# Optimization experiments

Measured on AMD Instinct MI355X. Metric: run time of the kernel, lower is better.

The kernel has to match this reference:

```python
import jax, jax.numpy as jnp
import numpy as np

B = 1 << 21          # shading points per batch
U_RES, CH = 400, 8   # spatial plane
A_RES, ACH = 50, 50 and 8  # placeholder, real consts below
A_RES, ACH = 50, 8   # angular planes (h/d)
HID = 32
IN_CH = CH + 2 * ACH  # 24


def _bilerp_clamp(tex, uv):
    # Bilinear interp, both axes clamped (U-plane). tex: (H,W,C), uv: (B,2) in [0,1]
    H, W, _ = tex.shape
    u = jnp.clip(uv[:, 0], 0.0, 1.0) * (W - 1)
    v = jnp.clip(uv[:, 1], 0.0, 1.0) * (H - 1)
    x0 = jnp.floor(u).astype(jnp.int32)
    x1 = jnp.clip(x0 + 1, 0, W - 1)
    y0 = jnp.floor(v).astype(jnp.int32)
    y1 = jnp.clip(y0 + 1, 0, H - 1)
    ur = (u - x0.astype(u.dtype))[:, None]
    vr = (v - y0.astype(v.dtype))[:, None]
    p00 = tex[y0, x0]; p10 = tex[y0, x1]; p01 = tex[y1, x0]; p11 = tex[y1, x1]
    return ((1 - ur) * (1 - vr) * p00 + ur * (1 - vr) * p10
            + (1 - ur) * vr * p01 + ur * vr * p11)


def _bilerp_wrap_u(tex, uv):
    # Bilinear interp wrapping the u (phi) axis, clamping v (H/D planes).
    H, W, _ = tex.shape
    u = (uv[:, 0] % 1.0) * W
    v = jnp.clip(uv[:, 1], 0.0, 1.0) * (H - 1)
    x0f = jnp.floor(u)
    x0 = x0f.astype(jnp.int32) % W
    x1 = (x0 + 1) % W
    y0 = jnp.floor(v).astype(jnp.int32)
    y1 = jnp.clip(y0 + 1, 0, H - 1)
    ur = (u - x0f)[:, None]
    vr = (v - y0.astype(v.dtype))[:, None]
    p00 = tex[y0, x0]; p10 = tex[y0, x1]; p01 = tex[y1, x0]; p11 = tex[y1, x1]
    return ((1 - ur) * (1 - vr) * p00 + ur * (1 - vr) * p10
            + (1 - ur) * vr * p01 + ur * vr * p11)


def setup_inputs() -> dict:
    key = jax.random.key(0)
    ks = jax.random.split(key, 8)
    x = jax.random.uniform(ks[0], (B, 6), dtype=jnp.float32)
    u_plane = 0.01 * jax.random.normal(ks[1], (U_RES, U_RES, CH), dtype=jnp.float32)
    h_plane = 0.01 * jax.random.normal(ks[2], (A_RES, A_RES, ACH), dtype=jnp.float32)
    d_plane = 0.01 * jax.random.normal(ks[3], (A_RES, A_RES, ACH), dtype=jnp.float32)
    def lin_w(k, fout, fin):  # torch nn.Linear default init (kaiming-uniform-ish)
        lim = 1.0 / np.sqrt(fin)
        return jax.random.uniform(k, (fout, fin), jnp.float32, -lim, lim)
    W0 = lin_w(ks[4], HID, IN_CH)
    W1 = lin_w(ks[5], HID, HID)
    W2 = lin_w(ks[6], HID, HID)
    W3 = lin_w(ks[7], 3, HID)
    return {"x": x, "u_plane": u_plane, "h_plane": h_plane, "d_plane": d_plane,
            "W0": W0, "W1": W1, "W2": W2, "W3": W3}


def reference(x, u_plane, h_plane, d_plane, W0, W1, W2, W3):
    # Split and reorder: H/D planes receive (u=phi, v=theta)
    uv = x[:, 0:2]
    h_uv = jnp.stack((x[:, 3], x[:, 2]), axis=1)
    d_uv = jnp.stack((x[:, 5], x[:, 4]), axis=1)
    fU = _bilerp_clamp(u_plane, uv)       # (B, CH)
    fH = _bilerp_wrap_u(h_plane, h_uv)    # (B, ACH)
    fD = _bilerp_wrap_u(d_plane, d_uv)    # (B, ACH)
    feat = jnp.concatenate([fU, fH, fD], axis=1)  # (B, 24)
    # Quant mode 'off' -> QLinear is a plain bias-free matmul with W^T
    h = jax.nn.relu(feat @ W0.T)
    h = jax.nn.relu(h @ W1.T)
    h = jax.nn.relu(h @ W2.T)
    return h @ W3.T  # (B, 3)
```

## Files before the change

kernel.cpp:

```cpp
#include <hip/hip_runtime.h>

typedef _Float16 half4 __attribute__((ext_vector_type(4)));
typedef _Float16 half8 __attribute__((ext_vector_type(8)));
typedef float floatx4 __attribute__((ext_vector_type(4)));

#define U_RESV 400
#define A_RESV 50

#define UHALVES (U_RESV * U_RESV * 8)
#define AHALVES (A_RESV * A_RESV * 8)
#define WOFF    (UHALVES + 2 * AHALVES)
#define W0OFF   0
#define W1OFF   896
#define W2OFF   2048
#define W3OFF   3200
#define WTOT    3776

__device__ __forceinline__ float clamp01(float x) { return fminf(fmaxf(x, 0.0f), 1.0f); }

__device__ __forceinline__ floatx4 mfma16(half4 a, half4 b, floatx4 c) {
    return __builtin_amdgcn_mfma_f32_16x16x16f16(a, b, c, 0, 0, 0);
}
__device__ __forceinline__ half4 zero4() {
    half4 h; h[0] = h[1] = h[2] = h[3] = (_Float16)0.f; return h;
}
__device__ __forceinline__ half4 relu4(half4 v) {
#if __has_builtin(__builtin_elementwise_max)
    return __builtin_elementwise_max(v, zero4());
#else
    half4 r;
#pragma unroll
    for (int i = 0; i < 4; ++i) r[i] = v[i] > (_Float16)0.f ? v[i] : (_Float16)0.f;
    return r;
#endif
}

__device__ __forceinline__ void cvt_chunk(const float* __restrict__ src,
                                          _Float16* __restrict__ dst, int i) {
    float4 a = *(const float4*)(src + (size_t)i * 8);
    float4 b = *(const float4*)(src + (size_t)i * 8 + 4);
    half8 h;
    h[0] = (_Float16)a.x; h[1] = (_Float16)a.y; h[2] = (_Float16)a.z; h[3] = (_Float16)a.w;
    h[4] = (_Float16)b.x; h[5] = (_Float16)b.y; h[6] = (_Float16)b.z; h[7] = (_Float16)b.w;
    *(half8*)(dst + (size_t)i * 8) = h;
}

__device__ __forceinline__ void wblob_fill(const float* __restrict__ W0,
                                           const float* __restrict__ W1,
                                           const float* __restrict__ W2,
                                           const float* __restrict__ W3,
                                           _Float16* __restrict__ w, int tid, int nthr) {
    for (int i = tid; i < WTOT; i += nthr) {
        float v;
        if (i < W1OFF) {
            int r = i / 28, c = i - r * 28;
            v = (c < 24) ? W0[r * 24 + c] : 0.f;
        } else if (i < W2OFF) {
            int j = i - W1OFF, r = j / 36, c = j - r * 36;
            v = (c < 32) ? W1[r * 32 + c] : 0.f;
        } else if (i < W3OFF) {
            int j = i - W2OFF, r = j / 36, c = j - r * 36;
            v = (c < 32) ? W2[r * 32 + c] : 0.f;
        } else {
            int j = i - W3OFF, r = j / 36, c = j - r * 36;
            v = (r < 3 && c < 32) ? W3[r * 32 + c] : 0.f;
        }
        w[i] = (_Float16)v;
    }
}

__global__ __launch_bounds__(256) void pconv_kernel(
    const float* __restrict__ u_plane, const float* __restrict__ h_plane,
    const float* __restrict__ d_plane, const float* __restrict__ W0,
    const float* __restrict__ W1, const float* __restrict__ W2,
    const float* __restrict__ W3, _Float16* __restrict__ dst) {
    const int gid = blockIdx.x * 256 + threadIdx.x;
    const int gsz = gridDim.x * 256;
    for (int i = gid; i < UHALVES / 8; i += gsz) cvt_chunk(u_plane, dst, i);
    for (int i = gid; i < AHALVES / 8; i += gsz) cvt_chunk(h_plane, dst + UHALVES, i);
    for (int i = gid; i < AHALVES / 8; i += gsz) cvt_chunk(d_plane, dst + UHALVES + AHALVES, i);
    if (blockIdx.x == 0) wblob_fill(W0, W1, W2, W3, dst + WOFF, threadIdx.x, 256);
}

__global__ __launch_bounds__(256) void wprep_kernel(
    const float* __restrict__ W0, const float* __restrict__ W1,
    const float* __restrict__ W2, const float* __restrict__ W3,
    _Float16* __restrict__ wdst) {
    wblob_fill(W0, W1, W2, W3, wdst, threadIdx.x, 256);
}


template <bool F16P>
__global__ __launch_bounds__(512, 2) void tpmlp_kernel(
    const float* __restrict__ x,
    const void* __restrict__ u_tex,
    const void* __restrict__ h_tex,
    const void* __restrict__ d_tex,
    const _Float16* __restrict__ wsw,
    float* __restrict__ out) {
    const int tid  = threadIdx.x;
    const int lane = tid & 63;
    const int wv   = tid >> 6;
    const int q    = lane >> 4;
    const int c15  = lane & 15;

    __shared__ __align__(16) _Float16 fl[512 * 28];
    __shared__ __align__(16) _Float16 wl[WTOT];

    const size_t P = (size_t)blockIdx.x * 512 + tid;
    const float2* xp = (const float2*)(x + P * 6);
    float2 p01v = xp[0], p23v = xp[1], p45v = xp[2];

    uint4 w_a;
    if (tid < 472) w_a = ((const uint4*)wsw)[tid];

    int oU0, oU1, oU2, oU3;  float uw00, uw10, uw01, uw11;
    {
        float u = clamp01(p01v.x) * (float)(U_RESV - 1);
        float v = clamp01(p01v.y) * (float)(U_RESV - 1);
        float x0f = floorf(u), y0f = floorf(v);
        int x0 = (int)x0f, y0 = (int)y0f;
        int x1 = min(x0 + 1, U_RESV - 1), y1 = min(y0 + 1, U_RESV - 1);
        float ur = u - x0f, vr = v - y0f;
        uw00 = (1.0f - ur) * (1.0f - vr); uw10 = ur * (1.0f - vr);
        uw01 = (1.0f - ur) * vr;          uw11 = ur * vr;
        oU0 = (y0 * U_RESV + x0) * 8;
        oU1 = (y0 * U_RESV + x1) * 8;
        oU2 = (y1 * U_RESV + x0) * 8;
        oU3 = (y1 * U_RESV + x1) * 8;
    }
    int oH0, oH1, oH2, oH3;  float hw00, hw10, hw01, hw11;
    {
        float uu = p23v.y, vv = p23v.x;
        float uf = uu - floorf(uu);
        float u = uf * (float)A_RESV;
        float v = clamp01(vv) * (float)(A_RESV - 1);
        float x0f = floorf(u), y0f = floorf(v);
        int x0 = (int)x0f;
        int x1 = x0 + 1; if (x1 == A_RESV) x1 = 0;
        int y0 = (int)y0f;
        int y1 = min(y0 + 1, A_RESV - 1);
        float ur = u - x0f, vr = v - y0f;
        hw00 = (1.0f - ur) * (1.0f - vr); hw10 = ur * (1.0f - vr);
        hw01 = (1.0f - ur) * vr;          hw11 = ur * vr;
        oH0 = (y0 * A_RESV + x0) * 8;
        oH1 = (y0 * A_RESV + x1) * 8;
        oH2 = (y1 * A_RESV + x0) * 8;
        oH3 = (y1 * A_RESV + x1) * 8;
    }
    int oD0, oD1, oD2, oD3;  float dw00, dw10, dw01, dw11;
    {
        float uu = p45v.y, vv = p45v.x;
        float uf = uu - floorf(uu);
        float u = uf * (float)A_RESV;
        float v = clamp01(vv) * (float)(A_RESV - 1);
        float x0f = floorf(u), y0f = floorf(v);
        int x0 = (int)x0f;
        int x1 = x0 + 1; if (x1 == A_RESV) x1 = 0;
        int y0 = (int)y0f;
        int y1 = min(y0 + 1, A_RESV - 1);
        float ur = u - x0f, vr = v - y0f;
        dw00 = (1.0f - ur) * (1.0f - vr); dw10 = ur * (1.0f - vr);
        dw01 = (1.0f - ur) * vr;          dw11 = ur * vr;
        oD0 = (y0 * A_RESV + x0) * 8;
        oD1 = (y0 * A_RESV + x1) * 8;
        oD2 = (y1 * A_RESV + x0) * 8;
        oD3 = (y1 * A_RESV + x1) * 8;
    }

    half8 gU0, gU1, gU2, gU3, gH0, gH1, gH2, gH3, gD0, gD1, gD2, gD3;
    float4 sU0, sU1, sU2, sU3, sH0, sH1, sH2, sH3, sD0, sD1, sD2, sD3;
    float4 rU0, rU1, rU2, rU3, rH0, rH1, rH2, rH3, rD0, rD1, rD2, rD3;
    if constexpr (F16P) {
        const _Float16* up = (const _Float16*)u_tex;
        const _Float16* hp = (const _Float16*)h_tex;
        const _Float16* dp = (const _Float16*)d_tex;
        gU0 = *(const half8*)(up + oU0);
        gU1 = *(const half8*)(up + oU1);
        gU2 = *(const half8*)(up + oU2);
        gU3 = *(const half8*)(up + oU3);
        gH0 = *(const half8*)(hp + oH0);
        gH1 = *(const half8*)(hp + oH1);
        gH2 = *(const half8*)(hp + oH2);
        gH3 = *(const half8*)(hp + oH3);
        gD0 = *(const half8*)(dp + oD0);
        gD1 = *(const half8*)(dp + oD1);
        gD2 = *(const half8*)(dp + oD2);
        gD3 = *(const half8*)(dp + oD3);
    } else {
        const float* up = (const float*)u_tex;
        const float* hp = (const float*)h_tex;
        const float* dp = (const float*)d_tex;
        sU0 = *(const float4*)(up + oU0); rU0 = *(const float4*)(up + oU0 + 4);
        sU1 = *(const float4*)(up + oU1); rU1 = *(const float4*)(up + oU1 + 4);
        sU2 = *(const float4*)(up + oU2); rU2 = *(const float4*)(up + oU2 + 4);
        sU3 = *(const float4*)(up + oU3); rU3 = *(const float4*)(up + oU3 + 4);
        sH0 = *(const float4*)(hp + oH0); rH0 = *(const float4*)(hp + oH0 + 4);
        sH1 = *(const float4*)(hp + oH1); rH1 = *(const float4*)(hp + oH1 + 4);
        sH2 = *(const float4*)(hp + oH2); rH2 = *(const float4*)(hp + oH2 + 4);
        sH3 = *(const float4*)(hp + oH3); rH3 = *(const float4*)(hp + oH3 + 4);
        sD0 = *(const float4*)(dp + oD0); rD0 = *(const float4*)(dp + oD0 + 4);
        sD1 = *(const float4*)(dp + oD1); rD1 = *(const float4*)(dp + oD1 + 4);
        sD2 = *(const float4*)(dp + oD2); rD2 = *(const float4*)(dp + oD2 + 4);
        sD3 = *(const float4*)(dp + oD3); rD3 = *(const float4*)(dp + oD3 + 4);
    }
    __builtin_amdgcn_sched_barrier(0);

    if (tid < 472) ((uint4*)wl)[tid] = w_a;
    asm volatile("s_waitcnt lgkmcnt(0)" ::: "memory");
    __builtin_amdgcn_s_barrier();

    float fU[8], fH[8], fD[8];
    if constexpr (F16P) {
#pragma unroll
        for (int i = 0; i < 8; ++i) {
            float r = (float)gU0[i] * uw00;
            r = fmaf((float)gU1[i], uw10, r);
            r = fmaf((float)gU2[i], uw01, r);
            r = fmaf((float)gU3[i], uw11, r);
            fU[i] = r;
        }
#pragma unroll
        for (int i = 0; i < 8; ++i) {
            float r = (float)gH0[i] * hw00;
            r = fmaf((float)gH1[i], hw10, r);
            r = fmaf((float)gH2[i], hw01, r);
            r = fmaf((float)gH3[i], hw11, r);
            fH[i] = r;
        }
#pragma unroll
        for (int i = 0; i < 8; ++i) {
            float r = (float)gD0[i] * dw00;
            r = fmaf((float)gD1[i], dw10, r);
            r = fmaf((float)gD2[i], dw01, r);
            r = fmaf((float)gD3[i], dw11, r);
            fD[i] = r;
        }
    } else {
        const float* a;
        const float* b;
        const float* c;
        const float* d;
#pragma unroll
        for (int i = 0; i < 8; ++i) {
            a = i < 4 ? (const float*)&sU0 : (const float*)&rU0;
            b = i < 4 ? (const float*)&sU1 : (const float*)&rU1;
            c = i < 4 ? (const float*)&sU2 : (const float*)&rU2;
            d = i < 4 ? (const float*)&sU3 : (const float*)&rU3;
            int k = i & 3;
            float r = a[k] * uw00;
            r = fmaf(b[k], uw10, r);
            r = fmaf(c[k], uw01, r);
            r = fmaf(d[k], uw11, r);
            fU[i] = r;
        }
#pragma unroll
        for (int i = 0; i < 8; ++i) {
            a = i < 4 ? (const float*)&sH0 : (const float*)&rH0;
            b = i < 4 ? (const float*)&sH1 : (const float*)&rH1;
            c = i < 4 ? (const float*)&sH2 : (const float*)&rH2;
            d = i < 4 ? (const float*)&sH3 : (const float*)&rH3;
            int k = i & 3;
            float r = a[k] * hw00;
            r = fmaf(b[k], hw10, r);
            r = fmaf(c[k], hw01, r);
            r = fmaf(d[k], hw11, r);
            fH[i] = r;
        }
#pragma unroll
        for (int i = 0; i < 8; ++i) {
            a = i < 4 ? (const float*)&sD0 : (const float*)&rD0;
            b = i < 4 ? (const float*)&sD1 : (const float*)&rD1;
            c = i < 4 ? (const float*)&sD2 : (const float*)&rD2;
            d = i < 4 ? (const float*)&sD3 : (const float*)&rD3;
            int k = i & 3;
            float r = a[k] * dw00;
            r = fmaf(b[k], dw10, r);
            r = fmaf(c[k], dw01, r);
            r = fmaf(d[k], dw11, r);
            fD[i] = r;
        }
    }

    {
        _Float16* row = fl + tid * 28;
        half8 hU, hH, hD;
#pragma unroll
        for (int i = 0; i < 8; ++i) {
            hU[i] = (_Float16)fU[i];
            hH[i] = (_Float16)fH[i];
            hD[i] = (_Float16)fD[i];
        }
        *(half8*)(row)      = hU;
        *(half8*)(row + 8)  = hH;
        *(half8*)(row + 16) = hD;
    }
    asm volatile("s_waitcnt lgkmcnt(0)" ::: "memory");
    __builtin_amdgcn_sched_barrier(0);

    floatx4 zf; zf[0] = 0.f; zf[1] = 0.f; zf[2] = 0.f; zf[3] = 0.f;
    const _Float16* wb = fl + (size_t)wv * 64 * 28;
    const _Float16* w0l = wl + W0OFF;
    const _Float16* w1l = wl + W1OFF;
    const _Float16* w2l = wl + W2OFF;
    const _Float16* w3l = wl + W3OFF;

    half4 b0[4], b1[4];
#pragma unroll
    for (int j = 0; j < 4; ++j) {
        const _Float16* r = wb + (size_t)(j * 16 + c15) * 28;
        b0[j] = *(const half4*)(r + q * 4);
        b1[j] = (q < 2) ? *(const half4*)(r + 16 + q * 4) : zero4();
    }

    floatx4 cc[2][4];
#pragma unroll
    for (int m = 0; m < 2; ++m) {
        half4 a0 = *(const half4*)(w0l + (size_t)(16 * m + c15) * 28 + q * 4);
        half4 a1 = (q < 2) ? *(const half4*)(w0l + (size_t)(16 * m + c15) * 28 + 16 + q * 4) : zero4();
#pragma unroll
        for (int j = 0; j < 4; ++j)
            cc[m][j] = mfma16(a1, b1[j], mfma16(a0, b0[j], zf));
    }
#pragma unroll
    for (int j = 0; j < 4; ++j) {
#pragma unroll
        for (int e = 0; e < 4; ++e) {
            b0[j][e] = (_Float16)cc[0][j][e];
            b1[j][e] = (_Float16)cc[1][j][e];
        }
        b0[j] = relu4(b0[j]);
        b1[j] = relu4(b1[j]);
    }

#pragma unroll
    for (int m = 0; m < 2; ++m) {
        half4 a0 = *(const half4*)(w1l + (size_t)(16 * m + c15) * 36 + q * 4);
        half4 a1 = *(const half4*)(w1l + (size_t)(16 * m + c15) * 36 + 16 + q * 4);
#pragma unroll
        for (int j = 0; j < 4; ++j)
            cc[m][j] = mfma16(a1, b1[j], mfma16(a0, b0[j], zf));
    }
#pragma unroll
    for (int j = 0; j < 4; ++j) {
#pragma unroll
        for (int e = 0; e < 4; ++e) {
            b0[j][e] = (_Float16)cc[0][j][e];
            b1[j][e] = (_Float16)cc[1][j][e];
        }
        b0[j] = relu4(b0[j]);
        b1[j] = relu4(b1[j]);
    }

#pragma unroll
    for (int m = 0; m < 2; ++m) {
        half4 a0 = *(const half4*)(w2l + (size_t)(16 * m + c15) * 36 + q * 4);
        half4 a1 = *(const half4*)(w2l + (size_t)(16 * m + c15) * 36 + 16 + q * 4);
#pragma unroll
        for (int j = 0; j < 4; ++j)
            cc[m][j] = mfma16(a1, b1[j], mfma16(a0, b0[j], zf));
    }
#pragma unroll
    for (int j = 0; j < 4; ++j) {
#pragma unroll
        for (int e = 0; e < 4; ++e) {
            b0[j][e] = (_Float16)cc[0][j][e];
            b1[j][e] = (_Float16)cc[1][j][e];
        }
        b0[j] = relu4(b0[j]);
        b1[j] = relu4(b1[j]);
    }

    floatx4 c3[4];
    {
        half4 a0 = *(const half4*)(w3l + (size_t)c15 * 36 + q * 4);
        half4 a1 = *(const half4*)(w3l + (size_t)c15 * 36 + 16 + q * 4);
#pragma unroll
        for (int j = 0; j < 4; ++j)
            c3[j] = mfma16(a1, b1[j], mfma16(a0, b0[j], zf));
    }

    if (lane < 16) {
        const size_t base = (size_t)blockIdx.x * 512 + (size_t)wv * 64;
#pragma unroll
        for (int j = 0; j < 4; ++j) {
            size_t p = base + (size_t)j * 16 + lane;
            float* o = out + p * 3;
            o[0] = c3[j][0];
            o[1] = c3[j][1];
            o[2] = c3[j][2];
        }
    }
}

extern "C" void kernel_launch(void* const* d_in, const int* in_sizes, int n_in,
                              void* d_out, int out_size, void* d_ws, size_t ws_size,
                              hipStream_t stream) {
    const float* x       = (const float*)d_in[0];
    const float* u_plane = (const float*)d_in[1];
    const float* h_plane = (const float*)d_in[2];
    const float* d_plane = (const float*)d_in[3];
    const float* W0      = (const float*)d_in[4];
    const float* W1      = (const float*)d_in[5];
    const float* W2      = (const float*)d_in[6];
    const float* W3      = (const float*)d_in[7];
    float* out = (float*)d_out;
    _Float16* wsw = (_Float16*)d_ws;

    int n = in_sizes[0] / 6;
    int grid = n / 512;

    const size_t need = ((size_t)WOFF + WTOT) * 2;
    if (ws_size >= need) {
        pconv_kernel<<<648, 256, 0, stream>>>(u_plane, h_plane, d_plane,
                                              W0, W1, W2, W3, wsw);
        tpmlp_kernel<true><<<grid, 512, 0, stream>>>(
            x, (const void*)wsw, (const void*)(wsw + UHALVES),
            (const void*)(wsw + UHALVES + AHALVES), wsw + WOFF, out);
    } else {
        wprep_kernel<<<1, 256, 0, stream>>>(W0, W1, W2, W3, wsw);
        tpmlp_kernel<false><<<grid, 512, 0, stream>>>(
            x, (const void*)u_plane, (const void*)h_plane, (const void*)d_plane,
            wsw, out);
    }
}
```

Baseline: 72.68 us.

## Process multiple 512-point tiles per block to amortize weight staging

Each block now loops over K=4 consecutive 512-point tiles, loading the packed MLP weights into shared memory once and reusing them across iterations. The grid is reduced by 4x and launch bounds relaxed to one block per CU minimum, with gather setup factored into helper functions. This trades per-block weight load and launch overhead for fewer resident blocks and less latency hiding of the texture gathers.

```diff
diff --git a/kernel.cpp b/kernel.cpp
--- a/kernel.cpp
+++ b/kernel.cpp
@@ -89,9 +89,59 @@
     wblob_fill(W0, W1, W2, W3, wdst, threadIdx.x, 256);
 }
 
-
-template <bool F16P>
-__global__ __launch_bounds__(512, 2) void tpmlp_kernel(
+struct GA { int o0, o1, o2, o3; float w00, w10, w01, w11; };
+
+__device__ __forceinline__ GA mkU(float ux, float uy) {
+    GA g;
+    float u = clamp01(ux) * (float)(U_RESV - 1);
+    float v = clamp01(uy) * (float)(U_RESV - 1);
+    float x0f = floorf(u), y0f = floorf(v);
+    int x0 = (int)x0f, y0 = (int)y0f;
+    int x1 = min(x0 + 1, U_RESV - 1), y1 = min(y0 + 1, U_RESV - 1);
+    float ur = u - x0f, vr = v - y0f;
+    g.w00 = (1.0f - ur) * (1.0f - vr); g.w10 = ur * (1.0f - vr);
+    g.w01 = (1.0f - ur) * vr;          g.w11 = ur * vr;
+    g.o0 = (y0 * U_RESV + x0) * 8;
+    g.o1 = (y0 * U_RESV + x1) * 8;
+    g.o2 = (y1 * U_RESV + x0) * 8;
+    g.o3 = (y1 * U_RESV + x1) * 8;
+    return g;
+}
+__device__ __forceinline__ GA mkA(float uu, float vv) {
+    GA g;
+    float uf = uu - floorf(uu);
+    float u = uf * (float)A_RESV;
+    float v = clamp01(vv) * (float)(A_RESV - 1);
+    float x0f = floorf(u), y0f = floorf(v);
+    int x0 = (int)x0f;
+    int x1 = x0 + 1; if (x1 == A_RESV) x1 = 0;
+    int y0 = (int)y0f;
+    int y1 = min(y0 + 1, A_RESV - 1);
+    float ur = u - x0f, vr = v - y0f;
+    g.w00 = (1.0f - ur) * (1.0f - vr); g.w10 = ur * (1.0f - vr);
+    g.w01 = (1.0f - ur) * vr;          g.w11 = ur * vr;
+    g.o0 = (y0 * A_RESV + x0) * 8;
+    g.o1 = (y0 * A_RESV + x1) * 8;
+    g.o2 = (y1 * A_RESV + x0) * 8;
+    g.o3 = (y1 * A_RESV + x1) * 8;
+    return g;
+}
+
+__device__ __forceinline__ void blend8(half8 a, half8 b, half8 c, half8 d,
+                                       const GA& g, float* f) {
+#pragma unroll
+    for (int i = 0; i < 8; ++i) {
+        float r = (float)a[i] * g.w00;
+        r = fmaf((float)b[i], g.w10, r);
+        r = fmaf((float)c[i], g.w01, r);
+        r = fmaf((float)d[i], g.w11, r);
+        f[i] = r;
+    }
+}
+
+
+template <bool F16P, int K>
+__global__ __launch_bounds__(512, 1) void tpmlp_kernel(
     const float* __restrict__ x,
     const void* __restrict__ u_tex,
     const void* __restrict__ h_tex,
@@ -107,288 +157,219 @@
     __shared__ __align__(16) _Float16 fl[512 * 28];
     __shared__ __align__(16) _Float16 wl[WTOT];
 
-    const size_t P = (size_t)blockIdx.x * 512 + tid;
-    const float2* xp = (const float2*)(x + P * 6);
-    float2 p01v = xp[0], p23v = xp[1], p45v = xp[2];
-
-    uint4 w_a;
-    if (tid < 472) w_a = ((const uint4*)wsw)[tid];
-
-    int oU0, oU1, oU2, oU3;  float uw00, uw10, uw01, uw11;
     {
-        float u = clamp01(p01v.x) * (float)(U_RESV - 1);
-        float v = clamp01(p01v.y) * (float)(U_RESV - 1);
-        float x0f = floorf(u), y0f = floorf(v);
-        int x0 = (int)x0f, y0 = (int)y0f;
-        int x1 = min(x0 + 1, U_RESV - 1), y1 = min(y0 + 1, U_RESV - 1);
-        float ur = u - x0f, vr = v - y0f;
-        uw00 = (1.0f - ur) * (1.0f - vr); uw10 = ur * (1.0f - vr);
-        uw01 = (1.0f - ur) * vr;          uw11 = ur * vr;
-        oU0 = (y0 * U_RESV + x0) * 8;
-        oU1 = (y0 * U_RESV + x1) * 8;
-        oU2 = (y1 * U_RESV + x0) * 8;
-        oU3 = (y1 * U_RESV + x1) * 8;
+        const uint4* src = (const uint4*)wsw;
+        uint4 w_a;
+        if (tid < 472) w_a = src[tid];
+        if (tid < 472) ((uint4*)wl)[tid] = w_a;
     }
-    int oH0, oH1, oH2, oH3;  float hw00, hw10, hw01, hw11;
-    {
-        float uu = p23v.y, vv = p23v.x;
-        float uf = uu - floorf(uu);
-        float u = uf * (float)A_RESV;
-        float v = clamp01(vv) * (float)(A_RESV - 1);
-        float x0f = floorf(u), y0f = floorf(v);
-        int x0 = (int)x0f;
-        int x1 = x0 + 1; if (x1 == A_RESV) x1 = 0;
-        int y0 = (int)y0f;
-        int y1 = min(y0 + 1, A_RESV - 1);
-        float ur = u - x0f, vr = v - y0f;
-        hw00 = (1.0f - ur) * (1.0f - vr); hw10 = ur * (1.0f - vr);
-        hw01 = (1.0f - ur) * vr;          hw11 = ur * vr;
-        oH0 = (y0 * A_RESV + x0) * 8;
-        oH1 = (y0 * A_RESV + x1) * 8;
-        oH2 = (y1 * A_RESV + x0) * 8;
-        oH3 = (y1 * A_RESV + x1) * 8;
-    }
-    int oD0, oD1, oD2, oD3;  float dw00, dw10, dw01, dw11;
-    {
-        float uu = p45v.y, vv = p45v.x;
-        float uf = uu - floorf(uu);
-        float u = uf * (float)A_RESV;
-        float v = clamp01(vv) * (float)(A_RESV - 1);
-        float x0f = floorf(u), y0f = floorf(v);
-        int x0 = (int)x0f;
-        int x1 = x0 + 1; if (x1 == A_RESV) x1 = 0;
-        int y0 = (int)y0f;
-        int y1 = min(y0 + 1, A_RESV - 1);
-        float ur = u - x0f, vr = v - y0f;
-        dw00 = (1.0f - ur) * (1.0f - vr); dw10 = ur * (1.0f - vr);
-        dw01 = (1.0f - ur) * vr;          dw11 = ur * vr;
-        oD0 = (y0 * A_RESV + x0) * 8;
-        oD1 = (y0 * A_RESV + x1) * 8;
-        oD2 = (y1 * A_RESV + x0) * 8;
-        oD3 = (y1 * A_RESV + x1) * 8;
-    }
-
-    half8 gU0, gU1, gU2, gU3, gH0, gH1, gH2, gH3, gD0, gD1, gD2, gD3;
-    float4 sU0, sU1, sU2, sU3, sH0, sH1, sH2, sH3, sD0, sD1, sD2, sD3;
-    float4 rU0, rU1, rU2, rU3, rH0, rH1, rH2, rH3, rD0, rD1, rD2, rD3;
-    if constexpr (F16P) {
-        const _Float16* up = (const _Float16*)u_tex;
-        const _Float16* hp = (const _Float16*)h_tex;
-        const _Float16* dp = (const _Float16*)d_tex;
-        gU0 = *(const half8*)(up + oU0);
-        gU1 = *(const half8*)(up + oU1);
-        gU2 = *(const half8*)(up + oU2);
-        gU3 = *(const half8*)(up + oU3);
-        gH0 = *(const half8*)(hp + oH0);
-        gH1 = *(const half8*)(hp + oH1);
-        gH2 = *(const half8*)(hp + oH2);
-        gH3 = *(const half8*)(hp + oH3);
-        gD0 = *(const half8*)(dp + oD0);
-        gD1 = *(const half8*)(dp + oD1);
-        gD2 = *(const half8*)(dp + oD2);
-        gD3 = *(const half8*)(dp + oD3);
-    } else {
-        const float* up = (const float*)u_tex;
-        const float* hp = (const float*)h_tex;
-        const float* dp = (const float*)d_tex;
-        sU0 = *(const float4*)(up + oU0); rU0 = *(const float4*)(up + oU0 + 4);
-        sU1 = *(const float4*)(up + oU1); rU1 = *(const float4*)(up + oU1 + 4);
-        sU2 = *(const float4*)(up + oU2); rU2 = *(const float4*)(up + oU2 + 4);
-        sU3 = *(const float4*)(up + oU3); rU3 = *(const float4*)(up + oU3 + 4);
-        sH0 = *(const float4*)(hp + oH0); rH0 = *(const float4*)(hp + oH0 + 4);
-        sH1 = *(const float4*)(hp + oH1); rH1 = *(const float4*)(hp + oH1 + 4);
-        sH2 = *(const float4*)(hp + oH2); rH2 = *(const float4*)(hp + oH2 + 4);
-        sH3 = *(const float4*)(hp + oH3); rH3 = *(const float4*)(hp + oH3 + 4);
-        sD0 = *(const float4*)(dp + oD0); rD0 = *(const float4*)(dp + oD0 + 4);
-        sD1 = *(const float4*)(dp + oD1); rD1 = *(const float4*)(dp + oD1 + 4);
-        sD2 = *(const float4*)(dp + oD2); rD2 = *(const float4*)(dp + oD2 + 4);
-        sD3 = *(const float4*)(dp + oD3); rD3 = *(const float4*)(dp + oD3 + 4);
-    }
-    __builtin_amdgcn_sched_barrier(0);
-
-    if (tid < 472) ((uint4*)wl)[tid] = w_a;
-    asm volatile("s_waitcnt lgkmcnt(0)" ::: "memory");
-    __builtin_amdgcn_s_barrier();
-
-    float fU[8], fH[8], fD[8];
-    if constexpr (F16P) {
-#pragma unroll
-        for (int i = 0; i < 8; ++i) {
-            float r = (float)gU0[i] * uw00;
-            r = fmaf((float)gU1[i], uw10, r);
-            r = fmaf((float)gU2[i], uw01, r);
-            r = fmaf((float)gU3[i], uw11, r);
-            fU[i] = r;
-        }
-#pragma unroll
-        for (int i = 0; i < 8; ++i) {
-            float r = (float)gH0[i] * hw00;
-            r = fmaf((float)gH1[i], hw10, r);
-            r = fmaf((float)gH2[i], hw01, r);
-            r = fmaf((float)gH3[i], hw11, r);
-            fH[i] = r;
-        }
-#pragma unroll
-        for (int i = 0; i < 8; ++i) {
-            float r = (float)gD0[i] * dw00;
-            r = fmaf((float)gD1[i], dw10, r);
-            r = fmaf((float)gD2[i], dw01, r);
-            r = fmaf((float)gD3[i], dw11, r);
-            fD[i] = r;
-        }
-    } else {
-        const float* a;
-        const float* b;
-        const float* c;
-        const float* d;
-#pragma unroll
-        for (int i = 0; i < 8; ++i) {
-            a = i < 4 ? (const float*)&sU0 : (const float*)&rU0;
-            b = i < 4 ? (const float*)&sU1 : (const float*)&rU1;
-            c = i < 4 ? (const float*)&sU2 : (const float*)&rU2;
-            d = i < 4 ? (const float*)&sU3 : (const float*)&rU3;
-            int k = i & 3;
-            float r = a[k] * uw00;
-            r = fmaf(b[k], uw10, r);
-            r = fmaf(c[k], uw01, r);
-            r = fmaf(d[k], uw11, r);
-            fU[i] = r;
-        }
-#pragma unroll
-        for (int i = 0; i < 8; ++i) {
-            a = i < 4 ? (const float*)&sH0 : (const float*)&rH0;
-            b = i < 4 ? (const float*)&sH1 : (const float*)&rH1;
-            c = i < 4 ? (const float*)&sH2 : (const float*)&rH2;
-            d = i < 4 ? (const float*)&sH3 : (const float*)&rH3;
-            int k = i & 3;
-            float r = a[k] * hw00;
-            r = fmaf(b[k], hw10, r);
-            r = fmaf(c[k], hw01, r);
-            r = fmaf(d[k], hw11, r);
-            fH[i] = r;
-        }
-#pragma unroll
-        for (int i = 0; i < 8; ++i) {
-            a = i < 4 ? (const float*)&sD0 : (const float*)&rD0;
-            b = i < 4 ? (const float*)&sD1 : (const float*)&rD1;
-            c = i < 4 ? (const float*)&sD2 : (const float*)&rD2;
-            d = i < 4 ? (const float*)&sD3 : (const float*)&rD3;
-            int k = i & 3;
-            float r = a[k] * dw00;
-            r = fmaf(b[k], dw10, r);
-            r = fmaf(c[k], dw01, r);
-            r = fmaf(d[k], dw11, r);
-            fD[i] = r;
-        }
-    }
-
-    {
-        _Float16* row = fl + tid * 28;
-        half8 hU, hH, hD;
-#pragma unroll
-        for (int i = 0; i < 8; ++i) {
-            hU[i] = (_Float16)fU[i];
-            hH[i] = (_Float16)fH[i];
-            hD[i] = (_Float16)fD[i];
-        }
-        *(half8*)(row)      = hU;
-        *(half8*)(row + 8)  = hH;
-        *(half8*)(row + 16) = hD;
-    }
-    asm volatile("s_waitcnt lgkmcnt(0)" ::: "memory");
-    __builtin_amdgcn_sched_barrier(0);
-
-    floatx4 zf; zf[0] = 0.f; zf[1] = 0.f; zf[2] = 0.f; zf[3] = 0.f;
-    const _Float16* wb = fl + (size_t)wv * 64 * 28;
+    __syncthreads();
+
+    const _Float16* wb  = fl + (size_t)wv * 64 * 28;
     const _Float16* w0l = wl + W0OFF;
     const _Float16* w1l = wl + W1OFF;
     const _Float16* w2l = wl + W2OFF;
     const _Float16* w3l = wl + W3OFF;
-
-    half4 b0[4], b1[4];
-#pragma unroll
-    for (int j = 0; j < 4; ++j) {
-        const _Float16* r = wb + (size_t)(j * 16 + c15) * 28;
-        b0[j] = *(const half4*)(r + q * 4);
-        b1[j] = (q < 2) ? *(const half4*)(r + 16 + q * 4) : zero4();
-    }
-
-    floatx4 cc[2][4];
-#pragma unroll
-    for (int m = 0; m < 2; ++m) {
-        half4 a0 = *(const half4*)(w0l + (size_t)(16 * m + c15) * 28 + q * 4);
-        half4 a1 = (q < 2) ? *(const half4*)(w0l + (size_t)(16 * m + c15) * 28 + 16 + q * 4) : zero4();
-#pragma unroll
-        for (int j = 0; j < 4; ++j)
-            cc[m][j] = mfma16(a1, b1[j], mfma16(a0, b0[j], zf));
-    }
-#pragma unroll
-    for (int j = 0; j < 4; ++j) {
-#pragma unroll
-        for (int e = 0; e < 4; ++e) {
-            b0[j][e] = (_Float16)cc[0][j][e];
-            b1[j][e] = (_Float16)cc[1][j][e];
-        }
-        b0[j] = relu4(b0[j]);
-        b1[j] = relu4(b1[j]);
-    }
-
-#pragma unroll
-    for (int m = 0; m < 2; ++m) {
-        half4 a0 = *(const half4*)(w1l + (size_t)(16 * m + c15) * 36 + q * 4);
-        half4 a1 = *(const half4*)(w1l + (size_t)(16 * m + c15) * 36 + 16 + q * 4);
-#pragma unroll
-        for (int j = 0; j < 4; ++j)
-            cc[m][j] = mfma16(a1, b1[j], mfma16(a0, b0[j], zf));
-    }
-#pragma unroll
-    for (int j = 0; j < 4; ++j) {
-#pragma unroll
-        for (int e = 0; e < 4; ++e) {
-            b0[j][e] = (_Float16)cc[0][j][e];
-            b1[j][e] = (_Float16)cc[1][j][e];
-        }
-        b0[j] = relu4(b0[j]);
-        b1[j] = relu4(b1[j]);
-    }
-
-#pragma unroll
-    for (int m = 0; m < 2; ++m) {
-        half4 a0 = *(const half4*)(w2l + (size_t)(16 * m + c15) * 36 + q * 4);
-        half4 a1 = *(const half4*)(w2l + (size_t)(16 * m + c15) * 36 + 16 + q * 4);
-#pragma unroll
-        for (int j = 0; j < 4; ++j)
-            cc[m][j] = mfma16(a1, b1[j], mfma16(a0, b0[j], zf));
-    }
-#pragma unroll
-    for (int j = 0; j < 4; ++j) {
-#pragma unroll
-        for (int e = 0; e < 4; ++e) {
-            b0[j][e] = (_Float16)cc[0][j][e];
-            b1[j][e] = (_Float16)cc[1][j][e];
-        }
-        b0[j] = relu4(b0[j]);
-        b1[j] = relu4(b1[j]);
-    }
-
-    floatx4 c3[4];
-    {
-        half4 a0 = *(const half4*)(w3l + (size_t)c15 * 36 + q * 4);
-        half4 a1 = *(const half4*)(w3l + (size_t)c15 * 36 + 16 + q * 4);
-#pragma unroll
-        for (int j = 0; j < 4; ++j)
-            c3[j] = mfma16(a1, b1[j], mfma16(a0, b0[j], zf));
-    }
-
-    if (lane < 16) {
-        const size_t base = (size_t)blockIdx.x * 512 + (size_t)wv * 64;
+    const size_t blkbase = (size_t)blockIdx.x * (512 * K);
+
+#pragma unroll 1
+    for (int it = 0; it < K; ++it) {
+        const size_t P = blkbase + (size_t)it * 512 + tid;
+
+        const float2* xp = (const float2*)(x + P * 6);
+        float2 p01v = xp[0], p23v = xp[1], p45v = xp[2];
+
+        GA gU = mkU(p01v.x, p01v.y);
+        GA gH = mkA(p23v.y, p23v.x);
+        GA gD = mkA(p45v.y, p45v.x);
+
+        half8 gU0, gU1, gU2, gU3, gH0, gH1, gH2, gH3, gD0, gD1, gD2, gD3;
+        float4 sU0, sU1, sU2, sU3, sH0, sH1, sH2, sH3, sD0, sD1, sD2, sD3;
+        float4 rU0, rU1, rU2, rU3, rH0, rH1, rH2, rH3, rD0, rD1, rD2, rD3;
+        if constexpr (F16P) {
+            const _Float16* up = (const _Float16*)u_tex;
+            const _Float16* hp = (const _Float16*)h_tex;
+            const _Float16* dp = (const _Float16*)d_tex;
+            gU0 = *(const half8*)(up + gU.o0);
+            gU1 = *(const half8*)(up + gU.o1);
+            gU2 = *(const half8*)(up + gU.o2);
+            gU3 = *(const half8*)(up + gU.o3);
+            gH0 = *(const half8*)(hp + gH.o0);
+            gH1 = *(const half8*)(hp + gH.o1);
+            gH2 = *(const half8*)(hp + gH.o2);
+            gH3 = *(const half8*)(hp + gH.o3);
+            gD0 = *(const half8*)(dp + gD.o0);
+            gD1 = *(const half8*)(dp + gD.o1);
+            gD2 = *(const half8*)(dp + gD.o2);
+            gD3 = *(const half8*)(dp + gD.o3);
+        } else {
+            const float* up = (const float*)u_tex;
+            const float* hp = (const float*)h_tex;
+            const float* dp = (const float*)d_tex;
+            sU0 = *(const float4*)(up + gU.o0); rU0 = *(const float4*)(up + gU.o0 + 4);
+            sU1 = *(const float4*)(up + gU.o1); rU1 = *(const float4*)(up + gU.o1 + 4);
+            sU2 = *(const float4*)(up + gU.o2); rU2 = *(const float4*)(up + gU.o2 + 4);
+            sU3 = *(const float4*)(up + gU.o3); rU3 = *(const float4*)(up + gU.o3 + 4);
+            sH0 = *(const float4*)(hp + gH.o0); rH0 = *(const float4*)(hp + gH.o0 + 4);
+            sH1 = *(const float4*)(hp + gH.o1); rH1 = *(const float4*)(hp + gH.o1 + 4);
+            sH2 = *(const float4*)(hp + gH.o2); rH2 = *(const float4*)(hp + gH.o2 + 4);
+            sH3 = *(const float4*)(hp + gH.o3); rH3 = *(const float4*)(hp + gH.o3 + 4);
+            sD0 = *(const float4*)(dp + gD.o0); rD0 = *(const float4*)(dp + gD.o0 + 4);
+            sD1 = *(const float4*)(dp + gD.o1); rD1 = *(const float4*)(dp + gD.o1 + 4);
+            sD2 = *(const float4*)(dp + gD.o2); rD2 = *(const float4*)(dp + gD.o2 + 4);
+            sD3 = *(const float4*)(dp + gD.o3); rD3 = *(const float4*)(dp + gD.o3 + 4);
+        }
+        __builtin_amdgcn_sched_barrier(0);
+
+        float fU[8], fH[8], fD[8];
+        if constexpr (F16P) {
+            blend8(gU0, gU1, gU2, gU3, gU, fU);
+            blend8(gH0, gH1, gH2, gH3, gH, fH);
+            blend8(gD0, gD1, gD2, gD3, gD, fD);
+        } else {
+#pragma unroll
+            for (int i = 0; i < 8; ++i) {
+                const float* a = i < 4 ? (const float*)&sU0 : (const float*)&rU0;
+                const float* b = i < 4 ? (const float*)&sU1 : (const float*)&rU1;
+                const float* c = i < 4 ? (const float*)&sU2 : (const float*)&rU2;
+                const float* d = i < 4 ? (const float*)&sU3 : (const float*)&rU3;
+                int k = i & 3;
+                float r = a[k] * gU.w00;
+                r = fmaf(b[k], gU.w10, r);
+                r = fmaf(c[k], gU.w01, r);
+                r = fmaf(d[k], gU.w11, r);
+                fU[i] = r;
+            }
+#pragma unroll
+            for (int i = 0; i < 8; ++i) {
+                const float* a = i < 4 ? (const float*)&sH0 : (const float*)&rH0;
+                const float* b = i < 4 ? (const float*)&sH1 : (const float*)&rH1;
+                const float* c = i < 4 ? (const float*)&sH2 : (const float*)&rH2;
+                const float* d = i < 4 ? (const float*)&sH3 : (const float*)&rH3;
+                int k = i & 3;
+                float r = a[k] * gH.w00;
+                r = fmaf(b[k], gH.w10, r);
+                r = fmaf(c[k], gH.w01, r);
+                r = fmaf(d[k], gH.w11, r);
+                fH[i] = r;
+            }
+#pragma unroll
+            for (int i = 0; i < 8; ++i) {
+                const float* a = i < 4 ? (const float*)&sD0 : (const float*)&rD0;
+                const float* b = i < 4 ? (const float*)&sD1 : (const float*)&rD1;
+                const float* c = i < 4 ? (const float*)&sD2 : (const float*)&rD2;
+                const float* d = i < 4 ? (const float*)&sD3 : (const float*)&rD3;
+                int k = i & 3;
+                float r = a[k] * gD.w00;
+                r = fmaf(b[k], gD.w10, r);
+                r = fmaf(c[k], gD.w01, r);
+                r = fmaf(d[k], gD.w11, r);
+                fD[i] = r;
+            }
+        }
+
+        {
+            _Float16* row = fl + tid * 28;
+            half8 hU, hH, hD;
+#pragma unroll
+            for (int i = 0; i < 8; ++i) {
+                hU[i] = (_Float16)fU[i];
+                hH[i] = (_Float16)fH[i];
+                hD[i] = (_Float16)fD[i];
+            }
+            *(half8*)(row)      = hU;
+            *(half8*)(row + 8)  = hH;
+            *(half8*)(row + 16) = hD;
+        }
+        asm volatile("s_waitcnt lgkmcnt(0)" ::: "memory");
+        __builtin_amdgcn_sched_barrier(0);
+
+        floatx4 zf; zf[0] = 0.f; zf[1] = 0.f; zf[2] = 0.f; zf[3] = 0.f;
+        half4 b0[4], b1[4];
 #pragma unroll
         for (int j = 0; j < 4; ++j) {
-            size_t p = base + (size_t)j * 16 + lane;
-            float* o = out + p * 3;
-            o[0] = c3[j][0];
-            o[1] = c3[j][1];
-            o[2] = c3[j][2];
+            const _Float16* r = wb + (size_t)(j * 16 + c15) * 28;
+            b0[j] = *(const half4*)(r + q * 4);
+            b1[j] = (q < 2) ? *(const half4*)(r + 16 + q * 4) : zero4();
+        }
+
+        floatx4 cc[2][4];
+#pragma unroll
+        for (int m = 0; m < 2; ++m) {
+            half4 a0 = *(const half4*)(w0l + (size_t)(16 * m + c15) * 28 + q * 4);
+            half4 a1 = (q < 2) ? *(const half4*)(w0l + (size_t)(16 * m + c15) * 28 + 16 + q * 4) : zero4();
+#pragma unroll
+            for (int j = 0; j < 4; ++j)
+                cc[m][j] = mfma16(a1, b1[j], mfma16(a0, b0[j], zf));
+        }
+#pragma unroll
+        for (int j = 0; j < 4; ++j) {
+#pragma unroll
+            for (int e = 0; e < 4; ++e) {
+                b0[j][e] = (_Float16)cc[0][j][e];
+                b1[j][e] = (_Float16)cc[1][j][e];
+            }
+            b0[j] = relu4(b0[j]);
+            b1[j] = relu4(b1[j]);
+        }
+
+#pragma unroll
+        for (int m = 0; m < 2; ++m) {
+            half4 a0 = *(const half4*)(w1l + (size_t)(16 * m + c15) * 36 + q * 4);
+            half4 a1 = *(const half4*)(w1l + (size_t)(16 * m + c15) * 36 + 16 + q * 4);
+#pragma unroll
+            for (int j = 0; j < 4; ++j)
+                cc[m][j] = mfma16(a1, b1[j], mfma16(a0, b0[j], zf));
+        }
+#pragma unroll
+        for (int j = 0; j < 4; ++j) {
+#pragma unroll
+            for (int e = 0; e < 4; ++e) {
+                b0[j][e] = (_Float16)cc[0][j][e];
+                b1[j][e] = (_Float16)cc[1][j][e];
+            }
+            b0[j] = relu4(b0[j]);
+            b1[j] = relu4(b1[j]);
+        }
+
+#pragma unroll
+        for (int m = 0; m < 2; ++m) {
+            half4 a0 = *(const half4*)(w2l + (size_t)(16 * m + c15) * 36 + q * 4);
+            half4 a1 = *(const half4*)(w2l + (size_t)(16 * m + c15) * 36 + 16 + q * 4);
+#pragma unroll
+            for (int j = 0; j < 4; ++j)
+                cc[m][j] = mfma16(a1, b1[j], mfma16(a0, b0[j], zf));
+        }
+#pragma unroll
+        for (int j = 0; j < 4; ++j) {
+#pragma unroll
+            for (int e = 0; e < 4; ++e) {
+                b0[j][e] = (_Float16)cc[0][j][e];
+                b1[j][e] = (_Float16)cc[1][j][e];
+            }
+            b0[j] = relu4(b0[j]);
+            b1[j] = relu4(b1[j]);
+        }
+
+        floatx4 c3[4];
+        {
+            half4 a0 = *(const half4*)(w3l + (size_t)c15 * 36 + q * 4);
+            half4 a1 = *(const half4*)(w3l + (size_t)c15 * 36 + 16 + q * 4);
+#pragma unroll
+            for (int j = 0; j < 4; ++j)
+                c3[j] = mfma16(a1, b1[j], mfma16(a0, b0[j], zf));
+        }
+
+        if (lane < 16) {
+            const size_t base = blkbase + (size_t)it * 512 + (size_t)wv * 64;
+#pragma unroll
+            for (int j = 0; j < 4; ++j) {
+                size_t p = base + (size_t)j * 16 + lane;
+                float* o = out + p * 3;
+                o[0] = c3[j][0];
+                o[1] = c3[j][1];
+                o[2] = c3[j][2];
+            }
         }
     }
 }
@@ -408,18 +389,20 @@
     _Float16* wsw = (_Float16*)d_ws;
 
     int n = in_sizes[0] / 6;
-    int grid = n / 512;
+    constexpr int K = 4;
 
     const size_t need = ((size_t)WOFF + WTOT) * 2;
     if (ws_size >= need) {
         pconv_kernel<<<648, 256, 0, stream>>>(u_plane, h_plane, d_plane,
                                               W0, W1, W2, W3, wsw);
-        tpmlp_kernel<true><<<grid, 512, 0, stream>>>(
+        int grid = n / (512 * K);
+        tpmlp_kernel<true, K><<<grid, 512, 0, stream>>>(
             x, (const void*)wsw, (const void*)(wsw + UHALVES),
             (const void*)(wsw + UHALVES + AHALVES), wsw + WOFF, out);
     } else {
         wprep_kernel<<<1, 256, 0, stream>>>(W0, W1, W2, W3, wsw);
-        tpmlp_kernel<false><<<grid, 512, 0, stream>>>(
+        int grid = n / (512 * K);
+        tpmlp_kernel<false, K><<<grid, 512, 0, stream>>>(
             x, (const void*)u_plane, (const void*)h_plane, (const void*)d_plane,
             wsw, out);
     }
```

After: 74.44 us. +2.4%, slower.
